# Performance work log

Hardware: AMD Instinct MI355X
Metric: run time of the kernel (lower is better)

The kernel has to match this reference:

```python
import jax, jax.numpy as jnp
import numpy as np

B, S, D, H = 16, 512, 512, 8
DH = D // H
EPS = 1e-5
NEG = -1.0e9


def _layernorm(v, g, b):
    mu = jnp.mean(v, axis=-1, keepdims=True)
    var = jnp.mean(jnp.square(v - mu), axis=-1, keepdims=True)
    return (v - mu) * jax.lax.rsqrt(var + EPS) * g + b


def setup_inputs() -> dict:
    key = jax.random.key(0)
    ks = jax.random.split(key, 12)
    sd = 1.0 / np.sqrt(D)
    return {
        "x": jax.random.normal(ks[0], (B, S, D), dtype=jnp.float32),
        "mask": jax.random.randint(ks[1], (B, S, S), 0, 2, dtype=jnp.int32),
        "ln_g": jnp.ones((D,), jnp.float32),
        "ln_b": jnp.zeros((D,), jnp.float32),
        "lna_g": jnp.ones((S,), jnp.float32),  # LayerNorm over attention scores (last dim = S = model_dim)
        "lna_b": jnp.zeros((S,), jnp.float32),
        "Wq": jax.random.uniform(ks[2], (D, D), jnp.float32, -sd, sd),
        "bq": jnp.zeros((D,), jnp.float32),
        "Wk": jax.random.uniform(ks[3], (D, D), jnp.float32, -sd, sd),
        "bk": jnp.zeros((D,), jnp.float32),
        "Wv": jax.random.uniform(ks[4], (D, D), jnp.float32, -sd, sd),
        "bv": jnp.zeros((D,), jnp.float32),
        "Wd": jax.random.uniform(ks[5], (D, D), jnp.float32, -sd, sd),
        "bd": jnp.zeros((D,), jnp.float32),
    }


def reference(x, mask, ln_g, ln_b, lna_g, lna_b, Wq, bq, Wk, bk, Wv, bv, Wd, bd):
    # pre-LN
    h = _layernorm(x, ln_g, ln_b)  # [B,S,D]
    # projections -> [B,H,S,DH]
    q = (h @ Wq + bq).reshape(B, S, H, DH).transpose(0, 2, 1, 3)
    k = (h @ Wk + bk).reshape(B, S, H, DH).transpose(0, 2, 1, 3)
    v = (h @ Wv + bv).reshape(B, S, H, DH).transpose(0, 2, 1, 3)
    # raw scores [B,H,S,S]
    scores = jnp.einsum("bhqd,bhkd->bhqk", q, k) / jnp.sqrt(jnp.asarray(DH, x.dtype))
    # non-standard: LayerNorm over the key axis of the score matrix
    scores = _layernorm(scores, lna_g, lna_b)
    # mask (broadcast over heads), then softmax
    scores = jnp.where(mask[:, None, :, :] == 0, jnp.asarray(NEG, x.dtype), scores)
    attn = jax.nn.softmax(scores, axis=-1)
    # dropout omitted (eval mode / deterministic reference)
    out = jnp.einsum("bhqk,bhkd->bhqd", attn, v)
    out = out.transpose(0, 2, 1, 3).reshape(B, S, D)
    out = out @ Wd + bd
    return out + x
```

## Files before the change

kernel.cpp:

```cpp
#include <hip/hip_runtime.h>
#include <hip/hip_bf16.h>
#include <stdint.h>


typedef __hip_bfloat16 bf16;
typedef __bf16 bf16x8 __attribute__((ext_vector_type(8)));
typedef float f32x4 __attribute__((ext_vector_type(4)));

#define MFMA16(a, b, c) __builtin_amdgcn_mfma_f32_16x16x32_bf16((a), (b), (c), 0, 0, 0)

static __device__ __forceinline__ bf16 f2b(float v) { return __float2bfloat16(v); }
static __device__ __forceinline__ bf16x8 ld8(const bf16* p) { return *(const bf16x8*)p; }
static __device__ __forceinline__ uint16_t f2bu(float v) {
  return __hip_bfloat16_raw(__float2bfloat16(v)).x;
}
static __device__ __forceinline__ float bu2f(uint32_t u) {
  union { uint32_t i; float f; } c;
  c.i = u << 16;
  return c.f;
}
static __device__ __forceinline__ void stage16(const bf16* g, bf16* l) {
  __builtin_amdgcn_global_load_lds(
      (const __attribute__((address_space(1))) void*)g,
      (__attribute__((address_space(3))) void*)l, 16, 0, 0);
}

__global__ __launch_bounds__(256) void prep(
    const float* __restrict__ x, const float* __restrict__ lng,
    const float* __restrict__ lnb, bf16* __restrict__ h,
    const int* __restrict__ mask, uint32_t* __restrict__ bits,
    const float* __restrict__ W0, const float* __restrict__ W1,
    const float* __restrict__ W2, const float* __restrict__ W3,
    bf16* __restrict__ T0, bf16* __restrict__ T1,
    bf16* __restrict__ T2, bf16* __restrict__ T3) {
  __shared__ float t[32][33];
  const int bid = blockIdx.x;
  const int tid = threadIdx.x;
  const int w = tid >> 6, lane = tid & 63;

  if (bid < 2048) {
    int row = bid * 4 + w;
    const float* xr = x + (size_t)row * 512 + lane * 8;
    float4 v0 = *(const float4*)xr;
    float4 v1 = *(const float4*)(xr + 4);
    float s  = v0.x + v0.y + v0.z + v0.w + v1.x + v1.y + v1.z + v1.w;
    float s2 = v0.x * v0.x + v0.y * v0.y + v0.z * v0.z + v0.w * v0.w +
               v1.x * v1.x + v1.y * v1.y + v1.z * v1.z + v1.w * v1.w;
#pragma unroll
    for (int m = 1; m < 64; m <<= 1) {
      s += __shfl_xor(s, m);
      s2 += __shfl_xor(s2, m);
    }
    float mean = s * (1.0f / 512.0f);
    float var = s2 * (1.0f / 512.0f) - mean * mean;
    float rstd = rsqrtf(var + 1e-5f);
    const float4 g0 = *(const float4*)(lng + lane * 8);
    const float4 g1 = *(const float4*)(lng + lane * 8 + 4);
    const float4 b0 = *(const float4*)(lnb + lane * 8);
    const float4 b1 = *(const float4*)(lnb + lane * 8 + 4);
    union { uint16_t u[8]; bf16x8 v; } o;
    o.u[0] = f2bu((v0.x - mean) * rstd * g0.x + b0.x);
    o.u[1] = f2bu((v0.y - mean) * rstd * g0.y + b0.y);
    o.u[2] = f2bu((v0.z - mean) * rstd * g0.z + b0.z);
    o.u[3] = f2bu((v0.w - mean) * rstd * g0.w + b0.w);
    o.u[4] = f2bu((v1.x - mean) * rstd * g1.x + b1.x);
    o.u[5] = f2bu((v1.y - mean) * rstd * g1.y + b1.y);
    o.u[6] = f2bu((v1.z - mean) * rstd * g1.z + b1.z);
    o.u[7] = f2bu((v1.w - mean) * rstd * g1.w + b1.w);
    *(bf16x8*)(h + (size_t)row * 512 + lane * 8) = o.v;
  } else if (bid < 6144) {
    size_t base = (size_t)(bid - 2048) * 1024 + w * 64 + lane;
#pragma unroll
    for (int it = 0; it < 4; it++) {
      size_t e = base + it * 256;
      int mv = mask[e];
      unsigned long long bal = __ballot(mv != 0);
      if (lane == 0) ((unsigned long long*)bits)[e >> 6] = bal;
    }
  } else {
    int tt = bid - 6144;
    int wsel = tt >> 8, rem = tt & 255;
    int n0 = (rem & 15) * 32, k0 = (rem >> 4) * 32;
    const float* src; bf16* dst;
    switch (wsel) {
      case 0: src = W0; dst = T0; break;
      case 1: src = W1; dst = T1; break;
      case 2: src = W2; dst = T2; break;
      default: src = W3; dst = T3; break;
    }
    int tx = tid & 31, ty = tid >> 5;
#pragma unroll
    for (int i = 0; i < 4; i++) {
      int kk = ty * 4 + i;
      t[kk][tx] = src[(k0 + kk) * 512 + n0 + tx];
    }
    __syncthreads();
#pragma unroll
    for (int i = 0; i < 4; i++) {
      int nn = ty * 4 + i;
      dst[(n0 + nn) * 512 + k0 + tx] = f2b(t[tx][nn]);
    }
  }
}

__global__ __launch_bounds__(256) void gemm_qkv(
    const bf16* __restrict__ hm,
    const bf16* __restrict__ WT0, const bf16* __restrict__ WT1, const bf16* __restrict__ WT2,
    const float* __restrict__ bq, const float* __restrict__ bk, const float* __restrict__ bv,
    bf16* __restrict__ outq, bf16* __restrict__ outk, bf16* __restrict__ outvT) {
  const int sel = blockIdx.z;
  const bf16* WT = sel == 0 ? WT0 : (sel == 1 ? WT1 : WT2);
  const float* bias = sel == 0 ? bq : (sel == 1 ? bk : bv);
  __shared__ __align__(16) uint16_t SM[128 * 136];
  bf16* buf = (bf16*)SM;
  int tid = threadIdx.x;
  int w = tid >> 6, lane = tid & 63, q4 = lane >> 4, l16 = lane & 15;
  int wr = w >> 1, wc = w & 1;
  int m0 = blockIdx.x * 128, n0 = blockIdx.y * 128;
  f32x4 acc[4][4];
#pragma unroll
  for (int i = 0; i < 4; i++)
#pragma unroll
    for (int j = 0; j < 4; j++) acc[i][j] = (f32x4){0.f, 0.f, 0.f, 0.f};

  const int srow = tid >> 2, sc8 = (tid & 3) * 8;
  const int srow1 = (256 + tid) >> 2, sc81 = ((256 + tid) & 3) * 8;

  {
    bf16* As = buf;
    bf16* Bs = buf + 4096;
    stage16(&hm[(size_t)(m0 + srow) * 512 + sc8], &As[(size_t)tid * 8]);
    stage16(&WT[(size_t)(n0 + srow) * 512 + sc8], &Bs[(size_t)tid * 8]);
    stage16(&hm[(size_t)(m0 + srow1) * 512 + sc81], &As[(size_t)(256 + tid) * 8]);
    stage16(&WT[(size_t)(n0 + srow1) * 512 + sc81], &Bs[(size_t)(256 + tid) * 8]);
  }

  int cur = 0;
  for (int kc = 0; kc < 16; kc++) {
    if (kc < 15) {
      int k0 = (kc + 1) * 32;
      bf16* As = buf + (cur ^ 1) * 8192;
      bf16* Bs = As + 4096;
      stage16(&hm[(size_t)(m0 + srow) * 512 + k0 + sc8], &As[(size_t)tid * 8]);
      stage16(&WT[(size_t)(n0 + srow) * 512 + k0 + sc8], &Bs[(size_t)tid * 8]);
      stage16(&hm[(size_t)(m0 + srow1) * 512 + k0 + sc81], &As[(size_t)(256 + tid) * 8]);
      stage16(&WT[(size_t)(n0 + srow1) * 512 + k0 + sc81], &Bs[(size_t)(256 + tid) * 8]);
      asm volatile("s_waitcnt vmcnt(4)" ::: "memory");
    } else {
      asm volatile("s_waitcnt vmcnt(0)" ::: "memory");
    }
    __builtin_amdgcn_s_barrier();
    __builtin_amdgcn_sched_barrier(0);
    {
      bf16* As = buf + cur * 8192;
      bf16* Bs = As + 4096;
      bf16x8 af[4], bfr[4];
#pragma unroll
      for (int rt = 0; rt < 4; rt++)
        af[rt] = ld8(&As[(wr * 64 + rt * 16 + l16) * 32 + q4 * 8]);
#pragma unroll
      for (int nt = 0; nt < 4; nt++)
        bfr[nt] = ld8(&Bs[(wc * 64 + nt * 16 + l16) * 32 + q4 * 8]);
#pragma unroll
      for (int rt = 0; rt < 4; rt++)
#pragma unroll
        for (int nt = 0; nt < 4; nt++) acc[rt][nt] = MFMA16(af[rt], bfr[nt], acc[rt][nt]);
    }
    __builtin_amdgcn_sched_barrier(0);
    __builtin_amdgcn_s_barrier();
    cur ^= 1;
  }

  if (sel != 2) {
    const float scale = sel == 0 ? 0.125f : 1.0f;
#pragma unroll
    for (int rt = 0; rt < 4; rt++)
#pragma unroll
      for (int nt = 0; nt < 4; nt++) {
        int ncol = wc * 64 + nt * 16 + l16;
        float bsv = bias[n0 + ncol];
#pragma unroll
        for (int r = 0; r < 4; r++) {
          int mrow = wr * 64 + rt * 16 + q4 * 4 + r;
          SM[mrow * 136 + ncol] = f2bu((acc[rt][nt][r] + bsv) * scale);
        }
      }
    __syncthreads();
    bf16* dst = sel == 0 ? outq : outk;
#pragma unroll
    for (int p = 0; p < 8; p++) {
      int e = p * 256 + tid;
      int row = e >> 4, c8 = (e & 15) * 8;
      bf16x8 vv = *(bf16x8*)&SM[row * 136 + c8];
      int gm = m0 + row, b_ = gm >> 9, s_ = gm & 511;
      int n = n0 + c8, hh = n >> 6, dh = n & 63;
      *(bf16x8*)(dst + ((size_t)((b_ * 8 + hh) * 512 + s_)) * 64 + dh) = vv;
    }
  } else {
#pragma unroll
    for (int rt = 0; rt < 4; rt++)
#pragma unroll
      for (int nt = 0; nt < 4; nt++) {
        int ncol = wc * 64 + nt * 16 + l16;
        float bsv = bias[n0 + ncol];
        union { uint16_t q[4]; uint2 u; } pk;
#pragma unroll
        for (int r = 0; r < 4; r++) pk.q[r] = f2bu(acc[rt][nt][r] + bsv);
        *(uint2*)&SM[ncol * 136 + wr * 64 + rt * 16 + q4 * 4] = pk.u;
      }
    __syncthreads();
#pragma unroll
    for (int p = 0; p < 8; p++) {
      int e = p * 256 + tid;
      int nn = e >> 4, s8 = (e & 15) * 8;
      bf16x8 vv = *(bf16x8*)&SM[nn * 136 + s8];
      int n = n0 + nn, hh = n >> 6, dh = n & 63;
      int gm = m0 + s8, b_ = gm >> 9, s_ = gm & 511;
      *(bf16x8*)(outvT + ((size_t)((b_ * 8 + hh) * 64 + dh)) * 512 + s_) = vv;
    }
  }
}

__global__ __launch_bounds__(256, 4) void attn_fused(
    const bf16* __restrict__ q, const bf16* __restrict__ k, const bf16* __restrict__ vT,
    const uint32_t* __restrict__ bits, const float* __restrict__ lg,
    const float* __restrict__ lb, bf16* __restrict__ ctx) {
  const int id = blockIdx.x;
  const int xcd = id & 7;
  const int j = id >> 3;
  const int mt = j & 7;
  const int bh = ((j >> 3) << 3) | xcd;
  const int m0 = mt * 64;
  const int b = bh >> 3, hh = bh & 7;
  const int tid = threadIdx.x;
  const int w = tid >> 6, lane = tid & 63, q4 = lane >> 4, l16 = lane & 15;

  __shared__ __align__(16) bf16 SBk[2][32 * 72];
  __shared__ __align__(16) bf16 SBv[2][64 * 40];
  __shared__ uint32_t GB[512];
  __shared__ uint32_t sbits[64][17];

  GB[tid] = (uint32_t)f2bu(lg[tid]) | ((uint32_t)f2bu(lb[tid]) << 16);
  GB[tid + 256] = (uint32_t)f2bu(lg[tid + 256]) | ((uint32_t)f2bu(lb[tid + 256]) << 16);
  {
    int row = tid >> 2, g = tid & 3;
    const uint32_t* src = bits + ((size_t)b * 512 + m0 + row) * 16 + g * 4;
    uint4 u = *(const uint4*)src;
    sbits[row][g * 4] = u.x; sbits[row][g * 4 + 1] = u.y;
    sbits[row][g * 4 + 2] = u.z; sbits[row][g * 4 + 3] = u.w;
  }

  const bf16* qb = q + ((size_t)bh * 512 + m0 + w * 16) * 64;
  const bf16* kb = k + (size_t)bh * 512 * 64;
  const bf16* vb = vT + (size_t)bh * 64 * 512;

  bf16x8 aq0 = ld8(qb + (size_t)l16 * 64 + q4 * 8);
  bf16x8 aq1 = ld8(qb + (size_t)l16 * 64 + 32 + q4 * 8);

  const int key0 = tid >> 3, dh8 = (tid & 7) * 8;
  const int dhv = tid >> 2, kk8 = (tid & 3) * 8;

  *(bf16x8*)&SBk[0][key0 * 72 + dh8] = ld8(kb + (size_t)key0 * 64 + dh8);
  __syncthreads();

  float s = 0.f, s2 = 0.f;
  for (int c = 0; c < 16; c++) {
    const int buf = c & 1;
    bf16x8 rk;
    if (c < 15) rk = ld8(kb + (size_t)((c + 1) * 32 + key0) * 64 + dh8);
    __builtin_amdgcn_s_setprio(1);
#pragma unroll
    for (int kg = 0; kg < 2; kg++) {
      const bf16* kp = &SBk[buf][(kg * 16 + l16) * 72];
      bf16x8 b0 = ld8(kp + q4 * 8);
      bf16x8 b1 = ld8(kp + 32 + q4 * 8);
      f32x4 acc = (f32x4){0.f, 0.f, 0.f, 0.f};
      acc = MFMA16(b0, aq0, acc);
      acc = MFMA16(b1, aq1, acc);
#pragma unroll
      for (int r = 0; r < 4; r++) {
        float v = acc[r];
        s += v;
        s2 += v * v;
      }
    }
    __builtin_amdgcn_s_setprio(0);
    if (c < 15)
      *(bf16x8*)&SBk[buf ^ 1][key0 * 72 + dh8] = rk;
    __syncthreads();
  }
  s += __shfl_xor(s, 16);  s += __shfl_xor(s, 32);
  s2 += __shfl_xor(s2, 16); s2 += __shfl_xor(s2, 32);
  const float mean = s * (1.0f / 512.0f);
  const float rstd = rsqrtf(s2 * (1.0f / 512.0f) - mean * mean + 1e-5f);

  *(bf16x8*)&SBk[0][key0 * 72 + dh8] = ld8(kb + (size_t)key0 * 64 + dh8);
  *(bf16x8*)&SBv[0][dhv * 40 + kk8] = ld8(vb + (size_t)dhv * 512 + kk8);
  __syncthreads();

  f32x4 o[4];
#pragma unroll
  for (int nt = 0; nt < 4; nt++) o[nt] = (f32x4){0.f, 0.f, 0.f, 0.f};
  float se = 0.f;
  const int src0 = ((q4 & 1) * 2) * 16 + l16;
  const int src1 = src0 + 16;
  const bool hi = (q4 >> 1) != 0;

  for (int c = 0; c < 16; c++) {
    const int buf = c & 1;
    bf16x8 rk, rv;
    if (c < 15) {
      rk = ld8(kb + (size_t)((c + 1) * 32 + key0) * 64 + dh8);
      rv = ld8(vb + (size_t)dhv * 512 + (c + 1) * 32 + kk8);
    }
    const uint32_t dw = sbits[w * 16 + l16][c];
    uint32_t Pk[2][2];
#pragma unroll
    for (int kg = 0; kg < 2; kg++) {
      const bf16* kp = &SBk[buf][(kg * 16 + l16) * 72];
      bf16x8 b0 = ld8(kp + q4 * 8);
      bf16x8 b1 = ld8(kp + 32 + q4 * 8);
      f32x4 acc = (f32x4){0.f, 0.f, 0.f, 0.f};
      __builtin_amdgcn_s_setprio(1);
      acc = MFMA16(b0, aq0, acc);
      acc = MFMA16(b1, aq1, acc);
      __builtin_amdgcn_s_setprio(0);
      uint4 gb4 = *(uint4*)&GB[c * 32 + kg * 16 + q4 * 4];
      uint16_t p[4];
#pragma unroll
      for (int r = 0; r < 4; r++) {
        uint32_t gb = r == 0 ? gb4.x : (r == 1 ? gb4.y : (r == 2 ? gb4.z : gb4.w));
        float t = (acc[r] - mean) * rstd * bu2f(gb & 0xffffu) + bu2f(gb >> 16);
        t = ((dw >> (kg * 16 + q4 * 4 + r)) & 1u) ? t : -1.0e9f;
        float pf = __expf(t);
        se += pf;
        p[r] = f2bu(pf);
      }
      Pk[kg][0] = (uint32_t)p[0] | ((uint32_t)p[1] << 16);
      Pk[kg][1] = (uint32_t)p[2] | ((uint32_t)p[3] << 16);
    }
    uint32_t t00 = __shfl(Pk[0][0], src0), t01 = __shfl(Pk[1][0], src0);
    uint32_t t10 = __shfl(Pk[0][1], src0), t11 = __shfl(Pk[1][1], src0);
    uint32_t t20 = __shfl(Pk[0][0], src1), t21 = __shfl(Pk[1][0], src1);
    uint32_t t30 = __shfl(Pk[0][1], src1), t31 = __shfl(Pk[1][1], src1);
    union { uint32_t d[4]; bf16x8 v; } af;
    af.d[0] = hi ? t01 : t00;
    af.d[1] = hi ? t11 : t10;
    af.d[2] = hi ? t21 : t20;
    af.d[3] = hi ? t31 : t30;
    __builtin_amdgcn_s_setprio(1);
#pragma unroll
    for (int nt = 0; nt < 4; nt++) {
      bf16x8 bv8 = ld8(&SBv[buf][(nt * 16 + l16) * 40 + q4 * 8]);
      o[nt] = MFMA16(af.v, bv8, o[nt]);
    }
    __builtin_amdgcn_s_setprio(0);
    if (c < 15) {
      *(bf16x8*)&SBk[buf ^ 1][key0 * 72 + dh8] = rk;
      *(bf16x8*)&SBv[buf ^ 1][dhv * 40 + kk8] = rv;
    }
    __syncthreads();
  }

  se += __shfl_xor(se, 16);
  se += __shfl_xor(se, 32);
  float invr = 1.0f / se;
  float inv[4];
#pragma unroll
  for (int r = 0; r < 4; r++) inv[r] = __shfl(invr, q4 * 4 + r);

  bf16* cb = ctx + ((size_t)b * 512 + m0 + w * 16) * 512 + hh * 64;
#pragma unroll
  for (int nt = 0; nt < 4; nt++)
#pragma unroll
    for (int r = 0; r < 4; r++)
      cb[(size_t)(q4 * 4 + r) * 512 + nt * 16 + l16] = f2b(o[nt][r] * inv[r]);
}

__global__ __launch_bounds__(256) void gemm_out(
    const bf16* __restrict__ ctx, const bf16* __restrict__ WT,
    const float* __restrict__ bd, const float* __restrict__ x, float* __restrict__ out) {
  __shared__ __align__(16) bf16 As[64 * 32];
  __shared__ __align__(16) bf16 Bs[128 * 32];
  int tid = threadIdx.x;
  int w = tid >> 6, lane = tid & 63, q4 = lane >> 4, l16 = lane & 15;
  int m0 = blockIdx.x * 64, n0 = blockIdx.y * 128;
  f32x4 acc[4][2];
#pragma unroll
  for (int i = 0; i < 4; i++)
#pragma unroll
    for (int j = 0; j < 2; j++) acc[i][j] = (f32x4){0.f, 0.f, 0.f, 0.f};

  for (int kc = 0; kc < 16; kc++) {
    int k0 = kc * 32;
    {
      int e = tid;
      int row = e >> 2, c8 = (e & 3) * 8;
      stage16(&ctx[(size_t)(m0 + row) * 512 + k0 + c8], &As[e * 8]);
    }
#pragma unroll
    for (int u0 = 0; u0 < 2; u0++) {
      int e = u0 * 256 + tid;
      int row = e >> 2, c8 = (e & 3) * 8;
      stage16(&WT[(size_t)(n0 + row) * 512 + k0 + c8], &Bs[e * 8]);
    }
    __syncthreads();
    bf16x8 af[4], bfr[2];
#pragma unroll
    for (int rt = 0; rt < 4; rt++)
      af[rt] = ld8(&As[(rt * 16 + l16) * 32 + q4 * 8]);
#pragma unroll
    for (int nt = 0; nt < 2; nt++)
      bfr[nt] = ld8(&Bs[(w * 32 + nt * 16 + l16) * 32 + q4 * 8]);
#pragma unroll
    for (int rt = 0; rt < 4; rt++)
#pragma unroll
      for (int nt = 0; nt < 2; nt++) acc[rt][nt] = MFMA16(af[rt], bfr[nt], acc[rt][nt]);
    __syncthreads();
  }
#pragma unroll
  for (int rt = 0; rt < 4; rt++) {
    int mbase = m0 + rt * 16 + q4 * 4;
#pragma unroll
    for (int nt = 0; nt < 2; nt++) {
      int n = n0 + w * 32 + nt * 16 + l16;
      float bsv = bd[n];
#pragma unroll
      for (int r = 0; r < 4; r++) {
        size_t idx = (size_t)(mbase + r) * 512 + n;
        out[idx] = acc[rt][nt][r] + bsv + x[idx];
      }
    }
  }
}

extern "C" void kernel_launch(void* const* d_in, const int* in_sizes, int n_in,
                              void* d_out, int out_size, void* d_ws, size_t ws_size,
                              hipStream_t stream) {
  const float* x = (const float*)d_in[0];
  const int* mask = (const int*)d_in[1];
  const float* ln_g = (const float*)d_in[2];
  const float* ln_b = (const float*)d_in[3];
  const float* lna_g = (const float*)d_in[4];
  const float* lna_b = (const float*)d_in[5];
  const float* Wq = (const float*)d_in[6];
  const float* bq = (const float*)d_in[7];
  const float* Wk = (const float*)d_in[8];
  const float* bk = (const float*)d_in[9];
  const float* Wv = (const float*)d_in[10];
  const float* bv = (const float*)d_in[11];
  const float* Wd = (const float*)d_in[12];
  const float* bd = (const float*)d_in[13];

  char* ws = (char*)d_ws;
  const size_t MB = 1024 * 1024;
  if (ws_size < 44 * MB) return;
  bf16* h = (bf16*)(ws);
  bf16* qd = (bf16*)(ws + 8 * MB);
  bf16* kd = (bf16*)(ws + 16 * MB);
  bf16* vTd = (bf16*)(ws + 24 * MB);
  bf16* ctx = (bf16*)(ws + 32 * MB);
  bf16* WqT = (bf16*)(ws + 40 * MB);
  bf16* WkT = (bf16*)(ws + 40 * MB + 512 * 1024);
  bf16* WvT = (bf16*)(ws + 40 * MB + 1024 * 1024);
  bf16* WdT = (bf16*)(ws + 40 * MB + 1536 * 1024);
  uint32_t* bits = (uint32_t*)(ws + 42 * MB);

  prep<<<7168, 256, 0, stream>>>(x, ln_g, ln_b, h, mask, bits,
                                 Wq, Wk, Wv, Wd, WqT, WkT, WvT, WdT);
  gemm_qkv<<<dim3(64, 4, 3), 256, 0, stream>>>(h, WqT, WkT, WvT, bq, bk, bv, qd, kd, vTd);
  attn_fused<<<1024, 256, 0, stream>>>(qd, kd, vTd, bits, lna_g, lna_b, ctx);
  gemm_out<<<dim3(128, 4), 256, 0, stream>>>(ctx, WdT, bd, x, (float*)d_out);
}
```

Measured before the change: 170.5 us.

## Double-buffer LDS staging in output projection GEMM to overlap loads with MFMA

The output-projection GEMM now uses two LDS buffers. It prefetches the next K-chunk of ctx and WT via global_load_lds while computing MFMAs on the current chunk, with explicit vmcnt waits and raw s_barrier in place of __syncthreads. This is meant to hide global-memory latency in a kernel that previously serialized load and compute each iteration. It doubles LDS use to 24 KB per block and relies on manual waitcnt and barrier ordering for correctness.

```diff
diff --git a/kernel.cpp b/kernel.cpp
--- a/kernel.cpp
+++ b/kernel.cpp
@@ -380,8 +380,7 @@
 __global__ __launch_bounds__(256) void gemm_out(
     const bf16* __restrict__ ctx, const bf16* __restrict__ WT,
     const float* __restrict__ bd, const float* __restrict__ x, float* __restrict__ out) {
-  __shared__ __align__(16) bf16 As[64 * 32];
-  __shared__ __align__(16) bf16 Bs[128 * 32];
+  __shared__ __align__(16) bf16 buf[2][6144];
   int tid = threadIdx.x;
   int w = tid >> 6, lane = tid & 63, q4 = lane >> 4, l16 = lane & 15;
   int m0 = blockIdx.x * 64, n0 = blockIdx.y * 128;
@@ -391,32 +390,51 @@
 #pragma unroll
     for (int j = 0; j < 2; j++) acc[i][j] = (f32x4){0.f, 0.f, 0.f, 0.f};
 
+  const int arow = tid >> 2, ac8 = (tid & 3) * 8;
+  const int brow0 = tid >> 2, bc80 = (tid & 3) * 8;
+  const int brow1 = (256 + tid) >> 2, bc81 = ((256 + tid) & 3) * 8;
+
+  {
+    bf16* As = buf[0];
+    bf16* Bs = buf[0] + 2048;
+    stage16(&ctx[(size_t)(m0 + arow) * 512 + ac8], &As[(size_t)tid * 8]);
+    stage16(&WT[(size_t)(n0 + brow0) * 512 + bc80], &Bs[(size_t)tid * 8]);
+    stage16(&WT[(size_t)(n0 + brow1) * 512 + bc81], &Bs[(size_t)(256 + tid) * 8]);
+  }
+
+  int cur = 0;
   for (int kc = 0; kc < 16; kc++) {
-    int k0 = kc * 32;
+    if (kc < 15) {
+      int k0 = (kc + 1) * 32;
+      bf16* As = buf[cur ^ 1];
+      bf16* Bs = As + 2048;
+      stage16(&ctx[(size_t)(m0 + arow) * 512 + k0 + ac8], &As[(size_t)tid * 8]);
+      stage16(&WT[(size_t)(n0 + brow0) * 512 + k0 + bc80], &Bs[(size_t)tid * 8]);
+      stage16(&WT[(size_t)(n0 + brow1) * 512 + k0 + bc81], &Bs[(size_t)(256 + tid) * 8]);
+      asm volatile("s_waitcnt vmcnt(3)" ::: "memory");
+    } else {
+      asm volatile("s_waitcnt vmcnt(0)" ::: "memory");
+    }
+    __builtin_amdgcn_s_barrier();
+    __builtin_amdgcn_sched_barrier(0);
     {
-      int e = tid;
-      int row = e >> 2, c8 = (e & 3) * 8;
-      stage16(&ctx[(size_t)(m0 + row) * 512 + k0 + c8], &As[e * 8]);
-    }
-#pragma unroll
-    for (int u0 = 0; u0 < 2; u0++) {
-      int e = u0 * 256 + tid;
-      int row = e >> 2, c8 = (e & 3) * 8;
-      stage16(&WT[(size_t)(n0 + row) * 512 + k0 + c8], &Bs[e * 8]);
-    }
-    __syncthreads();
-    bf16x8 af[4], bfr[2];
-#pragma unroll
-    for (int rt = 0; rt < 4; rt++)
-      af[rt] = ld8(&As[(rt * 16 + l16) * 32 + q4 * 8]);
-#pragma unroll
-    for (int nt = 0; nt < 2; nt++)
-      bfr[nt] = ld8(&Bs[(w * 32 + nt * 16 + l16) * 32 + q4 * 8]);
-#pragma unroll
-    for (int rt = 0; rt < 4; rt++)
-#pragma unroll
-      for (int nt = 0; nt < 2; nt++) acc[rt][nt] = MFMA16(af[rt], bfr[nt], acc[rt][nt]);
-    __syncthreads();
+      bf16* As = buf[cur];
+      bf16* Bs = As + 2048;
+      bf16x8 af[4], bfr[2];
+#pragma unroll
+      for (int rt = 0; rt < 4; rt++)
+        af[rt] = ld8(&As[(rt * 16 + l16) * 32 + q4 * 8]);
+#pragma unroll
+      for (int nt = 0; nt < 2; nt++)
+        bfr[nt] = ld8(&Bs[(w * 32 + nt * 16 + l16) * 32 + q4 * 8]);
+#pragma unroll
+      for (int rt = 0; rt < 4; rt++)
+#pragma unroll
+        for (int nt = 0; nt < 2; nt++) acc[rt][nt] = MFMA16(af[rt], bfr[nt], acc[rt][nt]);
+    }
+    __builtin_amdgcn_sched_barrier(0);
+    __builtin_amdgcn_s_barrier();
+    cur ^= 1;
   }
 #pragma unroll
   for (int rt = 0; rt < 4; rt++) {
```

Measured after the change: 169.8 us. About the same (-0.4%).
